# Kernel optimization log

Measured on AMD Instinct MI355X. Metric: run time of the kernel, lower is better.

## Reference

```python
import jax, jax.numpy as jnp
import numpy as np

N_NODES = 50000
N_EDGES = 800000


def setup_inputs() -> dict:
    key = jax.random.key(0)
    ks = jax.random.split(key, 6)
    x = jax.random.normal(ks[0], (N_NODES, 128), dtype=jnp.float32)
    edge_index = jax.random.randint(ks[1], (2, N_EDGES), 0, N_NODES, dtype=jnp.int64)
    # Glorot-ish scaled weights (PyG GCNConv uses glorot init)
    W1 = jax.random.normal(ks[2], (128, 256), dtype=jnp.float32) * (1.0 / np.sqrt(128))
    b1 = jnp.zeros((256,), dtype=jnp.float32)
    W2 = jax.random.normal(ks[3], (256, 128), dtype=jnp.float32) * (1.0 / np.sqrt(256))
    b2 = jnp.zeros((128,), dtype=jnp.float32)
    Wfc = jax.random.normal(ks[4], (128, 1), dtype=jnp.float32) * (1.0 / np.sqrt(128))
    bfc = jnp.zeros((1,), dtype=jnp.float32)
    return {"x": x, "edge_index": edge_index, "W1": W1, "b1": b1,
            "W2": W2, "b2": b2, "Wfc": Wfc, "bfc": bfc}


def _gcn_conv(x, src, dst, inv_sqrt_deg, W, b, n_nodes):
    # x: [N, Fin]; src/dst: [E+N] (self-loops included); W: [Fin, Fout]
    h = x @ W                                   # dense per-node transform
    norm = inv_sqrt_deg[src] * inv_sqrt_deg[dst]  # [E+N] symmetric normalization
    msg = h[src] * norm[:, None]                # gather + scale
    out = jax.ops.segment_sum(msg, dst, num_segments=n_nodes)  # scatter-add
    return out + b


def reference(x, edge_index, W1, b1, W2, b2, Wfc, bfc):
    n_nodes = x.shape[0]
    loops = jnp.arange(n_nodes, dtype=edge_index.dtype)
    src = jnp.concatenate([edge_index[0], loops])  # add self-loops (PyG default)
    dst = jnp.concatenate([edge_index[1], loops])
    deg = jax.ops.segment_sum(jnp.ones_like(dst, dtype=x.dtype), dst,
                              num_segments=n_nodes)  # in-degree incl. self-loop
    inv_sqrt_deg = jax.lax.rsqrt(deg)               # deg >= 1 due to self-loops

    h = jax.nn.relu(_gcn_conv(x, src, dst, inv_sqrt_deg, W1, b1, n_nodes))
    h = jax.nn.relu(_gcn_conv(h, src, dst, inv_sqrt_deg, W2, b2, n_nodes))
    pooled = jnp.mean(h, axis=0)                    # [output_dim]
    return pooled @ Wfc + bfc                       # [1]
```

## Files before the change

### kernel.cpp

```cpp
#include <hip/hip_runtime.h>


#define FEAT 128
#define TILE 16384
#define VPT  3

typedef __attribute__((ext_vector_type(8))) short short8;
typedef __attribute__((ext_vector_type(4))) float float4v;
typedef __attribute__((ext_vector_type(2))) float floatx2;

__device__ __forceinline__ unsigned int f2b(float f) {
    unsigned int u = __float_as_uint(f);
    return (u + 0x7fffu + ((u >> 16) & 1u)) >> 16;
}


__global__ __launch_bounds__(1024) void k_p1(const int* __restrict__ dst,
                                             int* __restrict__ cnt, int E, int B, int NW) {
    __shared__ int h[64];
    int t = threadIdx.x, w = blockIdx.x;
    if (t < B) h[t] = 0;
    __syncthreads();
    int e0 = w * TILE, e1 = min(e0 + TILE, E);
    for (int e = e0 + t; e < e1; e += 1024) atomicAdd(&h[dst[e] >> 10], 1);
    __syncthreads();
    if (t < B) cnt[t * NW + w] = h[t];
}

__global__ __launch_bounds__(1024) void k_bscan(int* __restrict__ cnt, int L) {
    __shared__ int s[1024];
    int t = threadIdx.x;
    int v[VPT]; int sum = 0;
#pragma unroll
    for (int j = 0; j < VPT; ++j) {
        int idx = t * VPT + j;
        int x = (idx < L) ? cnt[idx] : 0;
        v[j] = sum; sum += x;
    }
    s[t] = sum;
    __syncthreads();
    for (int d = 1; d < 1024; d <<= 1) {
        int x = (t >= d) ? s[t - d] : 0;
        __syncthreads();
        s[t] += x;
        __syncthreads();
    }
    int pre = (t > 0) ? s[t - 1] : 0;
#pragma unroll
    for (int j = 0; j < VPT; ++j) {
        int idx = t * VPT + j;
        if (idx < L) cnt[idx] = pre + v[j];
    }
}

__global__ __launch_bounds__(1024) void k_p3(const int* __restrict__ src,
                                             const int* __restrict__ dst,
                                             const int* __restrict__ cnt,
                                             unsigned int* __restrict__ ebuf,
                                             int E, int B, int NW) {
    __shared__ int cur[64];
    int t = threadIdx.x, w = blockIdx.x;
    if (t < B) cur[t] = cnt[t * NW + w];
    __syncthreads();
    int e0 = w * TILE, e1 = min(e0 + TILE, E);
    for (int e = e0 + t; e < e1; e += 1024) {
        int d = dst[e], s = src[e];
        int p = atomicAdd(&cur[d >> 10], 1);
        ebuf[p] = ((unsigned int)d << 16) | (unsigned int)s;
    }
}

__global__ __launch_bounds__(1024) void k_p4(const unsigned int* __restrict__ ebuf,
                                             const int* __restrict__ cnt,
                                             float* __restrict__ isd,
                                             int* __restrict__ off,
                                             unsigned short* __restrict__ csr,
                                             int E, int B, int NW, int N) {
    __shared__ int h[1024];
    __shared__ int s[1024];
    __shared__ int cur[1024];
    int t = threadIdx.x, b = blockIdx.x;
    h[t] = 0;
    __syncthreads();
    int s0 = cnt[b * NW];
    int s1 = (b + 1 < B) ? cnt[(b + 1) * NW] : E;
    for (int e = s0 + t; e < s1; e += 1024)
        atomicAdd(&h[(ebuf[e] >> 16) & 1023], 1);
    __syncthreads();
    int own = h[t];
    s[t] = own;
    __syncthreads();
    for (int d = 1; d < 1024; d <<= 1) {
        int x = (t >= d) ? s[t - d] : 0;
        __syncthreads();
        s[t] += x;
        __syncthreads();
    }
    int node = (b << 10) + t;
    int myoff = s0 + s[t] - own;
    cur[t] = myoff;
    if (node < N) {
        isd[node] = rsqrtf((float)(own + 1));
        off[node] = myoff;
        if (node == N - 1) off[N] = s0 + s[t];
    }
    __syncthreads();
    for (int e = s0 + t; e < s1; e += 1024) {
        unsigned int v = ebuf[e];
        int p = atomicAdd(&cur[(v >> 16) & 1023], 1);
        csr[p] = (unsigned short)(v & 0xffffu);
    }
}


__device__ __forceinline__ void wswz_one(const float* W, unsigned short* out,
                                         int N, int tid) {
    int lane = tid & 63, f = tid >> 6;
    int NT = N >> 4;
    int nt = f % NT, kt = f / NT;
    int m = lane & 15, quad = lane >> 4;
    short8 pk;
#pragma unroll
    for (int j = 0; j < 8; ++j)
        pk[j] = (short)f2b(W[(size_t)(kt * 32 + quad * 8 + j) * N + nt * 16 + m]);
    *(short8*)(out + (size_t)tid * 8) = pk;
}

__global__ void k_prep(const float* __restrict__ x, const float* __restrict__ isd,
                       unsigned int* __restrict__ xq, float* __restrict__ pooled,
                       const float* __restrict__ W1, unsigned short* __restrict__ w1z,
                       const float* __restrict__ W2, unsigned short* __restrict__ w2z,
                       int total4) {
    int i = blockIdx.x * blockDim.x + threadIdx.x;
    if (i < 8192) pooled[i] = 0.f;
    if (i < 4096) wswz_one(W1, w1z, 256, i);
    else if (i < 8192) wswz_one(W2, w2z, 128, i - 4096);
    if (i >= total4) return;
    float w = isd[i >> 5] * 16.f;
    float4 v = ((const float4*)x)[i];
    unsigned int u = __builtin_amdgcn_cvt_pk_fp8_f32(v.x * w, v.y * w, 0u, false);
    u = __builtin_amdgcn_cvt_pk_fp8_f32(v.z * w, v.w * w, u, true);
    xq[i] = u;
}


__device__ __forceinline__ void gather_row(const unsigned short* __restrict__ Xq,
                                           const int* __restrict__ off,
                                           const unsigned short* __restrict__ csr,
                                           int wid, int lane, float& ra0, float& ra1) {
    int beg = off[wid], end = off[wid + 1];
    float a0, a1;
    {
        unsigned int q = Xq[(size_t)wid * 64 + lane];
        floatx2 f = __builtin_amdgcn_cvt_pk_f32_fp8(q, false);
        a0 = f[0]; a1 = f[1];
    }
    int e = beg;
    for (; e + 8 <= end; e += 8) {
        int s0 = csr[e],     s1 = csr[e + 1], s2 = csr[e + 2], s3 = csr[e + 3];
        int s4 = csr[e + 4], s5 = csr[e + 5], s6 = csr[e + 6], s7 = csr[e + 7];
        unsigned int q0 = Xq[(size_t)s0 * 64 + lane];
        unsigned int q1 = Xq[(size_t)s1 * 64 + lane];
        unsigned int q2 = Xq[(size_t)s2 * 64 + lane];
        unsigned int q3 = Xq[(size_t)s3 * 64 + lane];
        unsigned int q4 = Xq[(size_t)s4 * 64 + lane];
        unsigned int q5 = Xq[(size_t)s5 * 64 + lane];
        unsigned int q6 = Xq[(size_t)s6 * 64 + lane];
        unsigned int q7 = Xq[(size_t)s7 * 64 + lane];
        floatx2 f0 = __builtin_amdgcn_cvt_pk_f32_fp8(q0, false);
        floatx2 f1 = __builtin_amdgcn_cvt_pk_f32_fp8(q1, false);
        floatx2 f2 = __builtin_amdgcn_cvt_pk_f32_fp8(q2, false);
        floatx2 f3 = __builtin_amdgcn_cvt_pk_f32_fp8(q3, false);
        floatx2 f4 = __builtin_amdgcn_cvt_pk_f32_fp8(q4, false);
        floatx2 f5 = __builtin_amdgcn_cvt_pk_f32_fp8(q5, false);
        floatx2 f6 = __builtin_amdgcn_cvt_pk_f32_fp8(q6, false);
        floatx2 f7 = __builtin_amdgcn_cvt_pk_f32_fp8(q7, false);
        a0 += f0[0] + f1[0] + f2[0] + f3[0] + f4[0] + f5[0] + f6[0] + f7[0];
        a1 += f0[1] + f1[1] + f2[1] + f3[1] + f4[1] + f5[1] + f6[1] + f7[1];
    }
    for (; e + 2 <= end; e += 2) {
        int s0 = csr[e], s1 = csr[e + 1];
        unsigned int q0 = Xq[(size_t)s0 * 64 + lane];
        unsigned int q1 = Xq[(size_t)s1 * 64 + lane];
        floatx2 f0 = __builtin_amdgcn_cvt_pk_f32_fp8(q0, false);
        floatx2 f1 = __builtin_amdgcn_cvt_pk_f32_fp8(q1, false);
        a0 += f0[0] + f1[0];
        a1 += f0[1] + f1[1];
    }
    if (e < end) {
        unsigned int q0 = Xq[(size_t)csr[e] * 64 + lane];
        floatx2 f0 = __builtin_amdgcn_cvt_pk_f32_fp8(q0, false);
        a0 += f0[0];
        a1 += f0[1];
    }
    ra0 = a0; ra1 = a1;
}


__global__ __launch_bounds__(256) void k_agg1(const unsigned short* __restrict__ Xq,
                                              const int* __restrict__ off,
                                              const unsigned short* __restrict__ csr,
                                              const float* __restrict__ isd,
                                              unsigned int* __restrict__ out, int n) {
    int wid  = (blockIdx.x * 256 + threadIdx.x) >> 6;
    int lane = threadIdx.x & 63;
    if (wid >= n) return;
    wid = __builtin_amdgcn_readfirstlane(wid);
    float a0, a1;
    gather_row(Xq, off, csr, wid, lane, a0, a1);
    float wn = isd[wid] * 0.0625f;
    out[(size_t)wid * 64 + lane] = f2b(wn * a0) | (f2b(wn * a1) << 16);
}


__global__ __launch_bounds__(256) void k_gemm12(const unsigned short* __restrict__ A,
                                                const unsigned short* __restrict__ W1z,
                                                const float* __restrict__ b1,
                                                const unsigned short* __restrict__ W2z,
                                                const float* __restrict__ isd,
                                                unsigned char* __restrict__ t2q, int M) {
    __shared__ unsigned short h1s[64 * 272];
    int tid = threadIdx.x;
    int lane = tid & 63, wm = tid >> 6;
    int m = lane & 15, quad = lane >> 4;

    long arow = (long)blockIdx.x * 64 + wm * 16 + m;
    if (arow >= M) arow = M - 1;
    const short8* Ap  = (const short8*)(A + (size_t)arow * 128);
    const short8* W1p = (const short8*)W1z + lane;

    float4v acc1[16];
    float4v zero = {0.f, 0.f, 0.f, 0.f};
#pragma unroll
    for (int nt = 0; nt < 16; ++nt) acc1[nt] = zero;
#pragma unroll
    for (int kt = 0; kt < 4; ++kt) {
        short8 a = Ap[kt * 4 + quad];
#pragma unroll
        for (int nt = 0; nt < 16; ++nt)
            acc1[nt] = __builtin_amdgcn_mfma_f32_16x16x32_bf16(a, W1p[(kt * 16 + nt) * 64],
                                                               acc1[nt], 0, 0, 0);
    }
    int r0 = wm * 16 + quad * 4;
#pragma unroll
    for (int nt = 0; nt < 16; ++nt) {
        int col = nt * 16 + m;
        float bz = b1[col];
#pragma unroll
        for (int reg = 0; reg < 4; ++reg) {
            float v = fmaxf(acc1[nt][reg] + bz, 0.f);
            h1s[(r0 + reg) * 272 + col] = (unsigned short)f2b(v);
        }
    }
    __syncthreads();

    float4v acc2[8];
#pragma unroll
    for (int nt = 0; nt < 8; ++nt) acc2[nt] = zero;
    const short8* W2p = (const short8*)W2z + lane;
    int rloc = wm * 16 + m;
#pragma unroll
    for (int kt = 0; kt < 8; ++kt) {
        short8 a2 = *(const short8*)(h1s + rloc * 272 + kt * 32 + quad * 8);
#pragma unroll
        for (int nt = 0; nt < 8; ++nt)
            acc2[nt] = __builtin_amdgcn_mfma_f32_16x16x32_bf16(a2, W2p[(kt * 8 + nt) * 64],
                                                               acc2[nt], 0, 0, 0);
    }
    int gr0 = blockIdx.x * 64 + wm * 16 + quad * 4;
    float sc[4];
#pragma unroll
    for (int reg = 0; reg < 4; ++reg) {
        int r = gr0 + reg;
        sc[reg] = ((r < M) ? isd[r] : 0.f) * 16.f;
    }
#pragma unroll
    for (int nt = 0; nt < 8; ++nt) {
        int col = nt * 16 + m;
#pragma unroll
        for (int reg = 0; reg < 4; ++reg) {
            int gr = gr0 + reg;
            if (gr < M) {
                float v = acc2[nt][reg] * sc[reg];
                unsigned int b = __builtin_amdgcn_cvt_pk_fp8_f32(v, v, 0u, false);
                t2q[(size_t)gr * 128 + col] = (unsigned char)(b & 0xffu);
            }
        }
    }
}


__global__ __launch_bounds__(256) void k_agg2p(const unsigned short* __restrict__ Xq,
                                               const int* __restrict__ off,
                                               const unsigned short* __restrict__ csr,
                                               const float* __restrict__ isd,
                                               const float* __restrict__ b2,
                                               float* __restrict__ pooled, int n) {
    __shared__ float s0[256], s1[256];
    int tid = threadIdx.x;
    int wid  = (blockIdx.x * 256 + tid) >> 6;
    int lane = tid & 63;
    float r0 = 0.f, r1 = 0.f;
    if (wid < n) {
        int wu = __builtin_amdgcn_readfirstlane(wid);
        float a0, a1;
        gather_row(Xq, off, csr, wu, lane, a0, a1);
        float wn = isd[wu] * 0.0625f;
        r0 = fmaxf(wn * a0 + b2[2 * lane], 0.f);
        r1 = fmaxf(wn * a1 + b2[2 * lane + 1], 0.f);
    }
    s0[tid] = r0;
    s1[tid] = r1;
    __syncthreads();
    if (tid < 64) {
        float t0 = s0[tid] + s0[tid + 64] + s0[tid + 128] + s0[tid + 192];
        float t1 = s1[tid] + s1[tid + 64] + s1[tid + 128] + s1[tid + 192];
        float* dst = pooled + (blockIdx.x & 63) * 128;
        atomicAdd(&dst[2 * tid], t0);
        atomicAdd(&dst[2 * tid + 1], t1);
    }
}


__global__ void k_final(const float* __restrict__ pooled,
                        const float* __restrict__ Wfc,
                        const float* __restrict__ bfc,
                        float* __restrict__ out, float invN) {
    __shared__ float s[128];
    int t = threadIdx.x;
    float v = 0.f;
#pragma unroll
    for (int r = 0; r < 64; ++r) v += pooled[r * 128 + t];
    s[t] = v * invN * Wfc[t];
    __syncthreads();
    for (int d = 64; d > 0; d >>= 1) {
        if (t < d) s[t] += s[t + d];
        __syncthreads();
    }
    if (t == 0) out[0] = s[0] + bfc[0];
}


extern "C" void kernel_launch(void* const* d_in, const int* in_sizes, int n_in,
                              void* d_out, int out_size, void* d_ws, size_t ws_size,
                              hipStream_t stream) {
    const float* x   = (const float*)d_in[0];
    const int*   ei  = (const int*)d_in[1];
    const float* W1  = (const float*)d_in[2];
    const float* b1  = (const float*)d_in[3];
    const float* W2  = (const float*)d_in[4];
    const float* b2  = (const float*)d_in[5];
    const float* Wfc = (const float*)d_in[6];
    const float* bfc = (const float*)d_in[7];
    float* out = (float*)d_out;

    int N = in_sizes[0] / FEAT;
    int E = in_sizes[1] / 2;
    const int* src = ei;
    const int* dst = ei + E;

    int NW = (E + TILE - 1) / TILE;
    int B  = (N + 1023) >> 10;

    char* p = (char*)d_ws;
    auto alloc = [&](size_t bytes) {
        char* r = p;
        p += (bytes + 255) & ~(size_t)255;
        return r;
    };
    int* cnt             = (int*)alloc((size_t)B * NW * 4);
    unsigned int* ebuf   = (unsigned int*)alloc((size_t)E * 4);
    unsigned short* csr  = (unsigned short*)alloc((size_t)E * 2);
    float* isd           = (float*)alloc((size_t)N * 4);
    int* off             = (int*)alloc((size_t)(N + 1) * 4);
    unsigned int* xq     = (unsigned int*)alloc((size_t)N * 32 * 4);
    unsigned int* agg1b  = (unsigned int*)alloc((size_t)N * 64 * 4);
    unsigned char* t2q   = (unsigned char*)alloc((size_t)N * 128);
    unsigned short* w1z  = (unsigned short*)alloc(128 * 256 * 2);
    unsigned short* w2z  = (unsigned short*)alloc(256 * 128 * 2);
    float* pooled        = (float*)alloc(64 * 128 * 4);

    k_p1<<<NW, 1024, 0, stream>>>(dst, cnt, E, B, NW);
    k_bscan<<<1, 1024, 0, stream>>>(cnt, B * NW);
    k_p3<<<NW, 1024, 0, stream>>>(src, dst, cnt, ebuf, E, B, NW);
    k_p4<<<B, 1024, 0, stream>>>(ebuf, cnt, isd, off, csr, E, B, NW, N);

    int total4 = N * FEAT / 4;
    k_prep<<<(total4 + 255) / 256, 256, 0, stream>>>(x, isd, xq, pooled,
                                                     W1, w1z, W2, w2z, total4);

    int gblk = (N + 63) / 64;
    int nblk = (N + 3) / 4;

    k_agg1<<<nblk, 256, 0, stream>>>((const unsigned short*)xq, off, csr, isd, agg1b, N);
    k_gemm12<<<gblk, 256, 0, stream>>>((const unsigned short*)agg1b, w1z, b1, w2z, isd, t2q, N);

    k_agg2p<<<nblk, 256, 0, stream>>>((const unsigned short*)t2q, off, csr, isd, b2,
                                      pooled, N);
    k_final<<<1, 128, 0, stream>>>(pooled, Wfc, bfc, out, 1.0f / (float)N);
}
```

Measured before the change: 214.2 us.

## Fuse first-layer neighbor aggregation into the two-layer GEMM kernel via LDS

The separate first-layer aggregation kernel is merged into the fused GEMM kernel. Each wave now gathers and normalizes its 16 rows directly into a shared-memory A tile instead of writing a bf16 intermediate to global memory that the GEMM kernel reads back. This removes one kernel launch and the global round trip of the N×128 bf16 buffer, and drops a block barrier that is no longer needed because each wave only reads rows it wrote itself. The cost is that the gather is now serialized over 16 rows per wave. With a larger LDS footprint per block, fewer waves are in flight to hide the latency of the irregular gathers.

```diff
diff --git a/kernel.cpp b/kernel.cpp
--- a/kernel.cpp
+++ b/kernel.cpp
@@ -197,45 +197,42 @@
 }
 
 
-__global__ __launch_bounds__(256) void k_agg1(const unsigned short* __restrict__ Xq,
+__global__ __launch_bounds__(256) void k_gg12(const unsigned short* __restrict__ Xq,
                                               const int* __restrict__ off,
                                               const unsigned short* __restrict__ csr,
+                                              const unsigned short* __restrict__ W1z,
+                                              const float* __restrict__ b1,
+                                              const unsigned short* __restrict__ W2z,
                                               const float* __restrict__ isd,
-                                              unsigned int* __restrict__ out, int n) {
-    int wid  = (blockIdx.x * 256 + threadIdx.x) >> 6;
-    int lane = threadIdx.x & 63;
-    if (wid >= n) return;
-    wid = __builtin_amdgcn_readfirstlane(wid);
-    float a0, a1;
-    gather_row(Xq, off, csr, wid, lane, a0, a1);
-    float wn = isd[wid] * 0.0625f;
-    out[(size_t)wid * 64 + lane] = f2b(wn * a0) | (f2b(wn * a1) << 16);
-}
-
-
-__global__ __launch_bounds__(256) void k_gemm12(const unsigned short* __restrict__ A,
-                                                const unsigned short* __restrict__ W1z,
-                                                const float* __restrict__ b1,
-                                                const unsigned short* __restrict__ W2z,
-                                                const float* __restrict__ isd,
-                                                unsigned char* __restrict__ t2q, int M) {
+                                              unsigned char* __restrict__ t2q, int M) {
+    __shared__ unsigned short As[64 * 136];
     __shared__ unsigned short h1s[64 * 272];
     int tid = threadIdx.x;
     int lane = tid & 63, wm = tid >> 6;
     int m = lane & 15, quad = lane >> 4;
 
-    long arow = (long)blockIdx.x * 64 + wm * 16 + m;
-    if (arow >= M) arow = M - 1;
-    const short8* Ap  = (const short8*)(A + (size_t)arow * 128);
+    int base = blockIdx.x * 64 + wm * 16;
+#pragma unroll 1
+    for (int rr = 0; rr < 16; ++rr) {
+        int row = base + rr;
+        if (row >= M) row = M - 1;
+        row = __builtin_amdgcn_readfirstlane(row);
+        float a0, a1;
+        gather_row(Xq, off, csr, row, lane, a0, a1);
+        float wn = isd[row] * 0.0625f;
+        unsigned int pk = f2b(wn * a0) | (f2b(wn * a1) << 16);
+        *(unsigned int*)(As + (wm * 16 + rr) * 136 + 2 * lane) = pk;
+    }
+
     const short8* W1p = (const short8*)W1z + lane;
-
     float4v acc1[16];
     float4v zero = {0.f, 0.f, 0.f, 0.f};
 #pragma unroll
     for (int nt = 0; nt < 16; ++nt) acc1[nt] = zero;
+    int arow_l = wm * 16 + m;
 #pragma unroll
     for (int kt = 0; kt < 4; ++kt) {
-        short8 a = Ap[kt * 4 + quad];
+        short8 a = *(const short8*)(As + arow_l * 136 + kt * 32 + quad * 8);
 #pragma unroll
         for (int nt = 0; nt < 16; ++nt)
             acc1[nt] = __builtin_amdgcn_mfma_f32_16x16x32_bf16(a, W1p[(kt * 16 + nt) * 64],
@@ -252,7 +249,6 @@
             h1s[(r0 + reg) * 272 + col] = (unsigned short)f2b(v);
         }
     }
-    __syncthreads();
 
     float4v acc2[8];
 #pragma unroll
@@ -374,7 +370,6 @@
     float* isd           = (float*)alloc((size_t)N * 4);
     int* off             = (int*)alloc((size_t)(N + 1) * 4);
     unsigned int* xq     = (unsigned int*)alloc((size_t)N * 32 * 4);
-    unsigned int* agg1b  = (unsigned int*)alloc((size_t)N * 64 * 4);
     unsigned char* t2q   = (unsigned char*)alloc((size_t)N * 128);
     unsigned short* w1z  = (unsigned short*)alloc(128 * 256 * 2);
     unsigned short* w2z  = (unsigned short*)alloc(256 * 128 * 2);
@@ -392,8 +387,8 @@
     int gblk = (N + 63) / 64;
     int nblk = (N + 3) / 4;
 
-    k_agg1<<<nblk, 256, 0, stream>>>((const unsigned short*)xq, off, csr, isd, agg1b, N);
-    k_gemm12<<<gblk, 256, 0, stream>>>((const unsigned short*)agg1b, w1z, b1, w2z, isd, t2q, N);
+    k_gg12<<<gblk, 256, 0, stream>>>((const unsigned short*)xq, off, csr,
+                                     w1z, b1, w2z, isd, t2q, N);
 
     k_agg2p<<<nblk, 256, 0, stream>>>((const unsigned short*)t2q, off, csr, isd, b2,
                                       pooled, N);
```

Result: slower. 255.3 us (+19.2%).

## Build CSR with global atomic degree histogram and direct scatter

Applied to the files above, without the earlier changes.

Replaces the two-level bucketed counting sort (per-tile bucket histograms, bucket scan, bucket scatter, per-bucket local sort) with a plain global-atomic degree histogram, a single-block scan over nodes, and a direct atomic scatter into the CSR array. This removes the intermediate edge buffer pass and two kernels, cutting memory traffic. In exchange it relies on global atomics into 50k counters, with contention and poor locality in the scatter, and a single-block serial-per-thread scan of about 49 elements each. Neighbor order within a row becomes nondeterministic, and zeroing pooled moves into a new zero kernel.

```diff
diff --git a/kernel.cpp b/kernel.cpp
--- a/kernel.cpp
+++ b/kernel.cpp
@@ -2,8 +2,6 @@
 
 
 #define FEAT 128
-#define TILE 16384
-#define VPT  3
 
 typedef __attribute__((ext_vector_type(8))) short short8;
 typedef __attribute__((ext_vector_type(4))) float float4v;
@@ -15,28 +13,30 @@
 }
 
 
-__global__ __launch_bounds__(1024) void k_p1(const int* __restrict__ dst,
-                                             int* __restrict__ cnt, int E, int B, int NW) {
-    __shared__ int h[64];
-    int t = threadIdx.x, w = blockIdx.x;
-    if (t < B) h[t] = 0;
-    __syncthreads();
-    int e0 = w * TILE, e1 = min(e0 + TILE, E);
-    for (int e = e0 + t; e < e1; e += 1024) atomicAdd(&h[dst[e] >> 10], 1);
-    __syncthreads();
-    if (t < B) cnt[t * NW + w] = h[t];
-}
-
-__global__ __launch_bounds__(1024) void k_bscan(int* __restrict__ cnt, int L) {
+__global__ __launch_bounds__(256) void k_zero(int* __restrict__ deg,
+                                              float* __restrict__ pooled, int N) {
+    int i = blockIdx.x * 256 + threadIdx.x;
+    if (i < N) deg[i] = 0;
+    if (i < 8192) pooled[i] = 0.f;
+}
+
+__global__ __launch_bounds__(256) void k_hist(const int* __restrict__ dst,
+                                              int* __restrict__ deg, int E) {
+    int i = blockIdx.x * 256 + threadIdx.x;
+    if (i < E) atomicAdd(&deg[dst[i]], 1);
+}
+
+__global__ __launch_bounds__(1024) void k_scan(const int* __restrict__ deg,
+                                               int* __restrict__ off,
+                                               int* __restrict__ cur,
+                                               float* __restrict__ isd,
+                                               int N, int VPTs) {
     __shared__ int s[1024];
     int t = threadIdx.x;
-    int v[VPT]; int sum = 0;
-#pragma unroll
-    for (int j = 0; j < VPT; ++j) {
-        int idx = t * VPT + j;
-        int x = (idx < L) ? cnt[idx] : 0;
-        v[j] = sum; sum += x;
-    }
+    int b0 = t * VPTs, b1 = min(b0 + VPTs, N);
+    if (b0 > N) b0 = N;
+    int sum = 0;
+    for (int i = b0; i < b1; ++i) sum += deg[i];
     s[t] = sum;
     __syncthreads();
     for (int d = 1; d < 1024; d <<= 1) {
@@ -45,70 +45,25 @@
         s[t] += x;
         __syncthreads();
     }
-    int pre = (t > 0) ? s[t - 1] : 0;
-#pragma unroll
-    for (int j = 0; j < VPT; ++j) {
-        int idx = t * VPT + j;
-        if (idx < L) cnt[idx] = pre + v[j];
-    }
-}
-
-__global__ __launch_bounds__(1024) void k_p3(const int* __restrict__ src,
-                                             const int* __restrict__ dst,
-                                             const int* __restrict__ cnt,
-                                             unsigned int* __restrict__ ebuf,
-                                             int E, int B, int NW) {
-    __shared__ int cur[64];
-    int t = threadIdx.x, w = blockIdx.x;
-    if (t < B) cur[t] = cnt[t * NW + w];
-    __syncthreads();
-    int e0 = w * TILE, e1 = min(e0 + TILE, E);
-    for (int e = e0 + t; e < e1; e += 1024) {
-        int d = dst[e], s = src[e];
-        int p = atomicAdd(&cur[d >> 10], 1);
-        ebuf[p] = ((unsigned int)d << 16) | (unsigned int)s;
-    }
-}
-
-__global__ __launch_bounds__(1024) void k_p4(const unsigned int* __restrict__ ebuf,
-                                             const int* __restrict__ cnt,
-                                             float* __restrict__ isd,
-                                             int* __restrict__ off,
-                                             unsigned short* __restrict__ csr,
-                                             int E, int B, int NW, int N) {
-    __shared__ int h[1024];
-    __shared__ int s[1024];
-    __shared__ int cur[1024];
-    int t = threadIdx.x, b = blockIdx.x;
-    h[t] = 0;
-    __syncthreads();
-    int s0 = cnt[b * NW];
-    int s1 = (b + 1 < B) ? cnt[(b + 1) * NW] : E;
-    for (int e = s0 + t; e < s1; e += 1024)
-        atomicAdd(&h[(ebuf[e] >> 16) & 1023], 1);
-    __syncthreads();
-    int own = h[t];
-    s[t] = own;
-    __syncthreads();
-    for (int d = 1; d < 1024; d <<= 1) {
-        int x = (t >= d) ? s[t - d] : 0;
-        __syncthreads();
-        s[t] += x;
-        __syncthreads();
-    }
-    int node = (b << 10) + t;
-    int myoff = s0 + s[t] - own;
-    cur[t] = myoff;
-    if (node < N) {
-        isd[node] = rsqrtf((float)(own + 1));
-        off[node] = myoff;
-        if (node == N - 1) off[N] = s0 + s[t];
-    }
-    __syncthreads();
-    for (int e = s0 + t; e < s1; e += 1024) {
-        unsigned int v = ebuf[e];
-        int p = atomicAdd(&cur[(v >> 16) & 1023], 1);
-        csr[p] = (unsigned short)(v & 0xffffu);
+    int run = (t > 0) ? s[t - 1] : 0;
+    for (int i = b0; i < b1; ++i) {
+        int dg = deg[i];
+        off[i] = run;
+        cur[i] = run;
+        isd[i] = rsqrtf((float)(dg + 1));
+        run += dg;
+    }
+    if (t == 0) off[N] = s[1023];
+}
+
+__global__ __launch_bounds__(256) void k_scatter(const int* __restrict__ src,
+                                                 const int* __restrict__ dst,
+                                                 int* __restrict__ cur,
+                                                 unsigned short* __restrict__ csr, int E) {
+    int i = blockIdx.x * 256 + threadIdx.x;
+    if (i < E) {
+        int p = atomicAdd(&cur[dst[i]], 1);
+        csr[p] = (unsigned short)src[i];
     }
 }
 
@@ -127,12 +82,11 @@
 }
 
 __global__ void k_prep(const float* __restrict__ x, const float* __restrict__ isd,
-                       unsigned int* __restrict__ xq, float* __restrict__ pooled,
+                       unsigned int* __restrict__ xq,
                        const float* __restrict__ W1, unsigned short* __restrict__ w1z,
                        const float* __restrict__ W2, unsigned short* __restrict__ w2z,
                        int total4) {
     int i = blockIdx.x * blockDim.x + threadIdx.x;
-    if (i < 8192) pooled[i] = 0.f;
     if (i < 4096) wswz_one(W1, w1z, 256, i);
     else if (i < 8192) wswz_one(W2, w2z, 128, i - 4096);
     if (i >= total4) return;
@@ -359,17 +313,14 @@
     const int* src = ei;
     const int* dst = ei + E;
 
-    int NW = (E + TILE - 1) / TILE;
-    int B  = (N + 1023) >> 10;
-
     char* p = (char*)d_ws;
     auto alloc = [&](size_t bytes) {
         char* r = p;
         p += (bytes + 255) & ~(size_t)255;
         return r;
     };
-    int* cnt             = (int*)alloc((size_t)B * NW * 4);
-    unsigned int* ebuf   = (unsigned int*)alloc((size_t)E * 4);
+    int* deg             = (int*)alloc((size_t)N * 4);
+    int* cur             = (int*)alloc((size_t)N * 4);
     unsigned short* csr  = (unsigned short*)alloc((size_t)E * 2);
     float* isd           = (float*)alloc((size_t)N * 4);
     int* off             = (int*)alloc((size_t)(N + 1) * 4);
@@ -380,14 +331,13 @@
     unsigned short* w2z  = (unsigned short*)alloc(256 * 128 * 2);
     float* pooled        = (float*)alloc(64 * 128 * 4);
 
-    k_p1<<<NW, 1024, 0, stream>>>(dst, cnt, E, B, NW);
-    k_bscan<<<1, 1024, 0, stream>>>(cnt, B * NW);
-    k_p3<<<NW, 1024, 0, stream>>>(src, dst, cnt, ebuf, E, B, NW);
-    k_p4<<<B, 1024, 0, stream>>>(ebuf, cnt, isd, off, csr, E, B, NW, N);
+    k_zero<<<(N + 255) / 256, 256, 0, stream>>>(deg, pooled, N);
+    k_hist<<<(E + 255) / 256, 256, 0, stream>>>(dst, deg, E);
+    k_scan<<<1, 1024, 0, stream>>>(deg, off, cur, isd, N, (N + 1023) / 1024);
+    k_scatter<<<(E + 255) / 256, 256, 0, stream>>>(src, dst, cur, csr, E);
 
     int total4 = N * FEAT / 4;
-    k_prep<<<(total4 + 255) / 256, 256, 0, stream>>>(x, isd, xq, pooled,
-                                                     W1, w1z, W2, w2z, total4);
+    k_prep<<<(total4 + 255) / 256, 256, 0, stream>>>(x, isd, xq, W1, w1z, W2, w2z, total4);
 
     int gblk = (N + 63) / 64;
     int nblk = (N + 3) / 4;
```

New measurement: 384.7 us. 1.8x slower.

## Shrink CSR build tiles and buckets, replace single-block scan with two-level scan

Applied to the files above, without the earlier changes.

Reduces the edge tile size from 16384 to 4096 and the destination bucket width from 1024 to 512 nodes. This raises the number of blocks in the counting, scatter and per-bucket CSR passes, giving more parallelism on the GPU. The larger count table no longer fits a single-block scan, so a two-level scan (per-block scan plus a tiny serial scan of block totals) is added, at the cost of one extra kernel launch. It also relies on the counts staying within 64 scan groups.

```diff
diff --git a/kernel.cpp b/kernel.cpp
--- a/kernel.cpp
+++ b/kernel.cpp
@@ -2,8 +2,9 @@
 
 
 #define FEAT 128
-#define TILE 16384
-#define VPT  3
+#define TILE 4096
+#define BSH  9
+#define BKN  512
 
 typedef __attribute__((ext_vector_type(8))) short short8;
 typedef __attribute__((ext_vector_type(4))) float float4v;
@@ -17,97 +18,108 @@
 
 __global__ __launch_bounds__(1024) void k_p1(const int* __restrict__ dst,
                                              int* __restrict__ cnt, int E, int B, int NW) {
-    __shared__ int h[64];
+    __shared__ int h[128];
     int t = threadIdx.x, w = blockIdx.x;
     if (t < B) h[t] = 0;
     __syncthreads();
     int e0 = w * TILE, e1 = min(e0 + TILE, E);
-    for (int e = e0 + t; e < e1; e += 1024) atomicAdd(&h[dst[e] >> 10], 1);
+    for (int e = e0 + t; e < e1; e += 1024) atomicAdd(&h[dst[e] >> BSH], 1);
     __syncthreads();
     if (t < B) cnt[t * NW + w] = h[t];
 }
 
-__global__ __launch_bounds__(1024) void k_bscan(int* __restrict__ cnt, int L) {
+__global__ __launch_bounds__(1024) void k_scanA(int* __restrict__ cnt,
+                                                int* __restrict__ tot, int L) {
     __shared__ int s[1024];
+    int t = threadIdx.x, g = blockIdx.x;
+    int i = g * 1024 + t;
+    int x = (i < L) ? cnt[i] : 0;
+    s[t] = x;
+    __syncthreads();
+    for (int d = 1; d < 1024; d <<= 1) {
+        int y = (t >= d) ? s[t - d] : 0;
+        __syncthreads();
+        s[t] += y;
+        __syncthreads();
+    }
+    if (i < L) cnt[i] = s[t] - x;
+    if (t == 1023) tot[g] = s[t];
+}
+
+__global__ void k_scanB(int* __restrict__ tot, int G) {
+    __shared__ int s[64];
     int t = threadIdx.x;
-    int v[VPT]; int sum = 0;
-#pragma unroll
-    for (int j = 0; j < VPT; ++j) {
-        int idx = t * VPT + j;
-        int x = (idx < L) ? cnt[idx] : 0;
-        v[j] = sum; sum += x;
-    }
-    s[t] = sum;
-    __syncthreads();
-    for (int d = 1; d < 1024; d <<= 1) {
-        int x = (t >= d) ? s[t - d] : 0;
-        __syncthreads();
-        s[t] += x;
-        __syncthreads();
-    }
-    int pre = (t > 0) ? s[t - 1] : 0;
-#pragma unroll
-    for (int j = 0; j < VPT; ++j) {
-        int idx = t * VPT + j;
-        if (idx < L) cnt[idx] = pre + v[j];
-    }
+    s[t] = (t < G) ? tot[t] : 0;
+    __syncthreads();
+    if (t == 0) {
+        int run = 0;
+        for (int g = 0; g < G; ++g) { int x = s[g]; s[g] = run; run += x; }
+    }
+    __syncthreads();
+    if (t < G) tot[t] = s[t];
 }
 
 __global__ __launch_bounds__(1024) void k_p3(const int* __restrict__ src,
                                              const int* __restrict__ dst,
                                              const int* __restrict__ cnt,
+                                             const int* __restrict__ tbase,
                                              unsigned int* __restrict__ ebuf,
                                              int E, int B, int NW) {
-    __shared__ int cur[64];
+    __shared__ int cur[128];
     int t = threadIdx.x, w = blockIdx.x;
-    if (t < B) cur[t] = cnt[t * NW + w];
+    if (t < B) { int i = t * NW + w; cur[t] = cnt[i] + tbase[i >> 10]; }
     __syncthreads();
     int e0 = w * TILE, e1 = min(e0 + TILE, E);
     for (int e = e0 + t; e < e1; e += 1024) {
         int d = dst[e], s = src[e];
-        int p = atomicAdd(&cur[d >> 10], 1);
+        int p = atomicAdd(&cur[d >> BSH], 1);
         ebuf[p] = ((unsigned int)d << 16) | (unsigned int)s;
     }
 }
 
 __global__ __launch_bounds__(1024) void k_p4(const unsigned int* __restrict__ ebuf,
                                              const int* __restrict__ cnt,
+                                             const int* __restrict__ tbase,
                                              float* __restrict__ isd,
                                              int* __restrict__ off,
                                              unsigned short* __restrict__ csr,
                                              int E, int B, int NW, int N) {
-    __shared__ int h[1024];
-    __shared__ int s[1024];
-    __shared__ int cur[1024];
+    __shared__ int h[BKN];
+    __shared__ int s[BKN];
+    __shared__ int cur[BKN];
     int t = threadIdx.x, b = blockIdx.x;
-    h[t] = 0;
-    __syncthreads();
-    int s0 = cnt[b * NW];
-    int s1 = (b + 1 < B) ? cnt[(b + 1) * NW] : E;
+    if (t < BKN) h[t] = 0;
+    __syncthreads();
+    int i0 = b * NW;
+    int s0 = cnt[i0] + tbase[i0 >> 10];
+    int s1 = E;
+    if (b + 1 < B) { int i1 = (b + 1) * NW; s1 = cnt[i1] + tbase[i1 >> 10]; }
     for (int e = s0 + t; e < s1; e += 1024)
-        atomicAdd(&h[(ebuf[e] >> 16) & 1023], 1);
-    __syncthreads();
-    int own = h[t];
-    s[t] = own;
-    __syncthreads();
-    for (int d = 1; d < 1024; d <<= 1) {
-        int x = (t >= d) ? s[t - d] : 0;
+        atomicAdd(&h[(ebuf[e] >> 16) & (BKN - 1)], 1);
+    __syncthreads();
+    int own = (t < BKN) ? h[t] : 0;
+    if (t < BKN) s[t] = own;
+    __syncthreads();
+    for (int d = 1; d < BKN; d <<= 1) {
+        int x = (t >= d && t < BKN) ? s[t - d] : 0;
         __syncthreads();
-        s[t] += x;
+        if (t < BKN) s[t] += x;
         __syncthreads();
     }
-    int node = (b << 10) + t;
-    int myoff = s0 + s[t] - own;
-    cur[t] = myoff;
-    if (node < N) {
-        isd[node] = rsqrtf((float)(own + 1));
-        off[node] = myoff;
-        if (node == N - 1) off[N] = s0 + s[t];
+    if (t < BKN) {
+        int node = (b << BSH) + t;
+        int myoff = s0 + s[t] - own;
+        cur[t] = myoff;
+        if (node < N) {
+            isd[node] = rsqrtf((float)(own + 1));
+            off[node] = myoff;
+            if (node == N - 1) off[N] = s0 + s[t];
+        }
     }
     __syncthreads();
     for (int e = s0 + t; e < s1; e += 1024) {
         unsigned int v = ebuf[e];
-        int p = atomicAdd(&cur[(v >> 16) & 1023], 1);
+        int p = atomicAdd(&cur[(v >> 16) & (BKN - 1)], 1);
         csr[p] = (unsigned short)(v & 0xffffu);
     }
 }
@@ -360,7 +372,9 @@
     const int* dst = ei + E;
 
     int NW = (E + TILE - 1) / TILE;
-    int B  = (N + 1023) >> 10;
+    int B  = (N + BKN - 1) >> BSH;
+    int L  = B * NW;
+    int G  = (L + 1023) / 1024;
 
     char* p = (char*)d_ws;
     auto alloc = [&](size_t bytes) {
@@ -368,7 +382,8 @@
         p += (bytes + 255) & ~(size_t)255;
         return r;
     };
-    int* cnt             = (int*)alloc((size_t)B * NW * 4);
+    int* cnt             = (int*)alloc((size_t)L * 4);
+    int* tot             = (int*)alloc(64 * 4);
     unsigned int* ebuf   = (unsigned int*)alloc((size_t)E * 4);
     unsigned short* csr  = (unsigned short*)alloc((size_t)E * 2);
     float* isd           = (float*)alloc((size_t)N * 4);
@@ -381,9 +396,10 @@
     float* pooled        = (float*)alloc(64 * 128 * 4);
 
     k_p1<<<NW, 1024, 0, stream>>>(dst, cnt, E, B, NW);
-    k_bscan<<<1, 1024, 0, stream>>>(cnt, B * NW);
-    k_p3<<<NW, 1024, 0, stream>>>(src, dst, cnt, ebuf, E, B, NW);
-    k_p4<<<B, 1024, 0, stream>>>(ebuf, cnt, isd, off, csr, E, B, NW, N);
+    k_scanA<<<G, 1024, 0, stream>>>(cnt, tot, L);
+    k_scanB<<<1, 64, 0, stream>>>(tot, G);
+    k_p3<<<NW, 1024, 0, stream>>>(src, dst, cnt, tot, ebuf, E, B, NW);
+    k_p4<<<B, 1024, 0, stream>>>(ebuf, cnt, tot, isd, off, csr, E, B, NW, N);
 
     int total4 = N * FEAT / 4;
     k_prep<<<(total4 + 255) / 256, 256, 0, stream>>>(x, isd, xq, pooled,
```

Result: faster. 199.6 us (-6.8%).
